# Kernel optimization log

Hardware: AMD Instinct MI355X
Metric: run time of the kernel (lower is better)

The kernel has to match this reference:

```python
import jax, jax.numpy as jnp
import numpy as np

B, L, H = 2, 512, 128

def setup_inputs() -> dict:
    key = jax.random.key(0)
    k1, k2, k3, _ = jax.random.split(key, 4)
    x = jax.random.normal(k1, (B, L, H), jnp.float32)
    y = jax.random.normal(k2, (B, L, H), jnp.float32)
    W_weight = jax.random.normal(k3, (H, 3 * H), jnp.float32) / np.sqrt(3 * H).astype(np.float32)
    W_bias = jnp.zeros((H,), jnp.float32)
    return {"x": x, "y": y, "W_weight": W_weight, "W_bias": W_bias}

def _span_max_context(x):
    """context[b,i,j,h] = max_{k=min(i,j)..max(i,j)} x[b,k,h], shape [B,L,L,H].
    Equivalent to the torch loop of diagonal running-max + symmetric scatter."""
    Bb, Ll, Hh = x.shape
    neg = jnp.full((Bb, 1, Hh), -jnp.inf, x.dtype)
    x_pad = jnp.concatenate([x, neg], axis=1)              # [B,L+1,H]
    d = jnp.arange(Ll)[:, None]                            # diagonal offset
    j = jnp.arange(Ll)[None, :]                            # start position
    shift_idx = jnp.minimum(d + j, Ll)                     # [L,L]; L -> -inf pad
    X2 = x_pad[:, shift_idx, :]                            # X2[b,d,j] = x[b,j+d]
    D = jax.lax.cummax(X2, axis=1)                         # D[b,d,j] = max_{k=j..j+d} x[b,k]
    i = jnp.arange(Ll)[:, None]
    jj = jnp.arange(Ll)[None, :]
    off = jnp.abs(i - jj)                                  # |i-j|
    lo = jnp.minimum(i, jj)                                # min(i,j)
    return D[:, off, lo, :]                                # [B,L,L,H]

def reference(x, y, W_weight, W_bias):
    Hh = x.shape[-1]
    ctx = _span_max_context(x)
    # Split W over the concat [x_i, y_j, context_ij] to avoid a [B,L,L,3H] intermediate.
    Wx, Wy, Wc = W_weight[:, :Hh], W_weight[:, Hh:2 * Hh], W_weight[:, 2 * Hh:]
    t = (jnp.einsum('blh,gh->blg', x, Wx)[:, :, None, :]
         + jnp.einsum('blh,gh->blg', y, Wy)[:, None, :, :]
         + jnp.einsum('bijh,gh->bijg', ctx, Wc)
         + W_bias)
    return jax.nn.gelu(t, approximate=False)               # [B,L,L,H]
```

## Files before the change

kernel.cpp:

```cpp
#include <hip/hip_runtime.h>
#include <hip/hip_bf16.h>

#define LL 512
#define HH 128
#define NBATCH 2
#define NT 32
#define NOFF (NT*(NT-1)/2)

typedef float f32x4 __attribute__((ext_vector_type(4)));
typedef short s16x8 __attribute__((ext_vector_type(8)));
typedef unsigned int u32x4 __attribute__((ext_vector_type(4)));

__device__ __forceinline__ unsigned short f2bfu(float f){
  __hip_bfloat16 h = __float2bfloat16(f);
  return __builtin_bit_cast(unsigned short, h);
}
__device__ __forceinline__ unsigned int bmax2(unsigned int a, unsigned int b){
  float lo = fmaxf(__uint_as_float(a << 16), __uint_as_float(b << 16));
  float hi = fmaxf(__uint_as_float(a & 0xFFFF0000u), __uint_as_float(b & 0xFFFF0000u));
  return __float_as_uint(hi) | (__float_as_uint(lo) >> 16);
}
__device__ __forceinline__ unsigned int packbf2(float lo, float hi){
  return ((__float_as_uint(hi) + 0x8000u) & 0xFFFF0000u)
       | ((__float_as_uint(lo) + 0x8000u) >> 16);
}
__device__ __forceinline__ u32x4 bmax4(u32x4 a, u32x4 b){
  u32x4 r; r[0]=bmax2(a[0],b[0]); r[1]=bmax2(a[1],b[1]);
  r[2]=bmax2(a[2],b[2]); r[3]=bmax2(a[3],b[3]); return r;
}
__device__ __forceinline__ float gelu_f(float v){
  float inner = v * fmaf(0.044715f, v*v, 1.0f);
  float e = __expf(1.5957691216f * inner);
  float s = __fdividef(1.0f, e + 1.0f);
  return fmaf(-v, s, v);
}
__device__ __forceinline__ f32x4 gelu4(f32x4 v){
  f32x4 r;
  #pragma unroll
  for (int i=0;i<4;++i) r[i] = gelu_f(v[i]);
  return r;
}

__global__ void prep_kernel(const float* __restrict__ x, const float* __restrict__ y,
                            const float* __restrict__ W, const float* __restrict__ bias,
                            float* __restrict__ t1, float* __restrict__ t2,
                            float* __restrict__ bmax, short* __restrict__ Wcb){
  int blk = blockIdx.x, tid = threadIdx.x;
  if (blk < NBATCH*LL){
    int b = blk >> 9, l = blk & (LL-1);
    __shared__ float xs[HH], ys[HH];
    size_t base = ((size_t)b*LL + l)*HH;
    if (tid < HH) xs[tid] = x[base + tid];
    else          ys[tid-HH] = y[base + tid - HH];
    __syncthreads();
    int role = tid >> 7, g = tid & (HH-1);
    const float4* wr = (const float4*)(W + (size_t)g*384 + role*HH);
    const float4* vs = (const float4*)(role ? ys : xs);
    float sA = 0.f, sB = 0.f;
    #pragma unroll
    for (int q=0;q<32;q+=2){
      float4 a = vs[q],   w1 = wr[q];
      sA = fmaf(a.x,w1.x, fmaf(a.y,w1.y, fmaf(a.z,w1.z, fmaf(a.w,w1.w, sA))));
      float4 c = vs[q+1], w2 = wr[q+1];
      sB = fmaf(c.x,w2.x, fmaf(c.y,w2.y, fmaf(c.z,w2.z, fmaf(c.w,w2.w, sB))));
    }
    float s = sA + sB;
    if (role == 0) t1[base + g] = s + bias[g];
    else           t2[base + g] = s;
  } else if (blk < NBATCH*LL + NBATCH*NT/2){
    int e = (blk - NBATCH*LL)*2 + (tid >> 7);
    int h = tid & (HH-1);
    int b = e >> 5, t = e & 31;
    float m = -INFINITY;
    #pragma unroll
    for (int r=0;r<16;++r) m = fmaxf(m, x[((size_t)b*LL + t*16 + r)*HH + h]);
    bmax[(size_t)e*HH + h] = m;
  } else {
    int e0 = ((blk - (NBATCH*LL + NBATCH*NT/2))*256 + tid)*8;
    #pragma unroll
    for (int i=0;i<8;++i){
      int e = e0 + i; int g = e >> 7, h = e & (HH-1);
      Wcb[e] = (short)f2bfu(W[(size_t)g*384 + 256 + h]);
    }
  }
}

__global__ __launch_bounds__(256, 4) void ctx_kernel(
    const float* __restrict__ x, const float* __restrict__ t1,
    const float* __restrict__ t2, const float* __restrict__ bmax,
    const short* __restrict__ Wcb, float* __restrict__ out)
{
  __shared__ __align__(16) unsigned int shs[8192];
  const int tid = threadIdx.x;
  const int b = blockIdx.y;
  const int w = tid >> 6, l = tid & 63, l16 = l & 15, lhi = l >> 4;
  const size_t bL = (size_t)b*LL;
  float* Bw = (float*)shs + w*1024;
  unsigned short* sIU = (unsigned short*)(shs + 4096);
  unsigned short* sJU = sIU + 2048;
  unsigned short* M   = (unsigned short*)(shs + 4096);

  const bool isdiag = (blockIdx.x >= NOFF);
  int ti, tj;
  if (!isdiag){
    int rem = blockIdx.x; ti = 0;
    while (rem >= NT-1-ti){ rem -= NT-1-ti; ++ti; }
    tj = ti + 1 + rem;
  } else { ti = tj = blockIdx.x - NOFF; }

  if (!isdiag){
    int role = tid >> 7, h = tid & (HH-1);
    if (role == 0){
      const float* xp = x + (bL + ti*16)*HH + h;
      float run = -INFINITY;
      #pragma unroll
      for (int r=15;r>=0;--r){ run = fmaxf(run, xp[r*HH]);
        sIU[r*HH + (h ^ ((r&7)<<3))] = f2bfu(run); }
    } else {
      const float* bp = bmax + ((size_t)b*NT)*HH + h;
      float run = -INFINITY;
      for (int t=ti+1;t<tj;++t) run = fmaxf(run, bp[t*HH]);
      const float* xp = x + (bL + tj*16)*HH + h;
      #pragma unroll
      for (int r=0;r<16;++r){ run = fmaxf(run, xp[r*HH]);
        sJU[r*HH + (h ^ ((r&7)<<3))] = f2bfu(run); }
    }
    __syncthreads();
  } else {
    { int e = tid*8; int r = e >> 7, h0 = e & (HH-1);
      const float* xp = x + (bL + ti*16 + r)*HH + h0;
      f32x4 v0 = *(const f32x4*)xp, v1 = *(const f32x4*)(xp+4);
      u32x4 pk; pk[0]=packbf2(v0[0],v0[1]); pk[1]=packbf2(v0[2],v0[3]);
      pk[2]=packbf2(v1[0],v1[1]); pk[3]=packbf2(v1[2],v1[3]);
      *(u32x4*)&M[r*HH + (h0 ^ ((r&7)<<3))] = pk;
    }
    __syncthreads();
    #pragma unroll
    for (int k=1;k<4;++k){
      int e = tid*8; int r = e >> 7, h0 = e & (HH-1);
      int r2 = min(r + (1<<(k-1)), 15);
      u32x4 a = *(const u32x4*)&M[((k-1)*16 + r )*HH + (h0 ^ ((r &7)<<3))];
      u32x4 c = *(const u32x4*)&M[((k-1)*16 + r2)*HH + (h0 ^ ((r2&7)<<3))];
      *(u32x4*)&M[(k*16 + r)*HH + (h0 ^ ((r&7)<<3))] = bmax4(a, c);
      __syncthreads();
    }
  }

  const int i0 = ti*16, j0 = tj*16;

  #pragma unroll
  for (int ps=0; ps<2; ++ps){
    const int ptA = w*4 + ps*2;
    u32x4 fr[2][4];
    if (!isdiag){
      #pragma unroll
      for (int s=0;s<2;++s){
        int pt = ptA + s;
        #pragma unroll
        for (int kb=0;kb<4;++kb){
          int h0 = kb*32 + lhi*8;
          u32x4 si = *(const u32x4*)&sIU[pt*HH + (h0 ^ ((pt&7)<<3))];
          u32x4 pj = *(const u32x4*)&sJU[l16*HH + (h0 ^ ((l16&7)<<3))];
          fr[s][kb] = bmax4(si, pj);
        }
      }
    } else {
      #pragma unroll
      for (int s=0;s<2;++s){
        int pt = ptA + s;
        int a = min(pt, l16), bb2 = max(pt, l16);
        int len = bb2 - a + 1;
        int k = 31 - __clz(len); if (k>3) k=3;
        int r2 = bb2 + 1 - (1<<k);
        #pragma unroll
        for (int kb=0;kb<4;++kb){
          int h0 = kb*32 + lhi*8;
          u32x4 ua = *(const u32x4*)&M[(k*16+a )*HH + (h0 ^ ((a &7)<<3))];
          u32x4 ub = *(const u32x4*)&M[(k*16+r2)*HH + (h0 ^ ((r2&7)<<3))];
          fr[s][kb] = bmax4(ua, ub);
        }
      }
    }

    #pragma unroll
    for (int q4=0; q4<4; ++q4){
      #pragma unroll
      for (int hf=0; hf<2; ++hf){
        const int nt = q4*2 + hf;
        s16x8 wcf[4];
        #pragma unroll
        for (int kb=0;kb<4;++kb)
          wcf[kb] = *(const s16x8*)(Wcb + (size_t)(nt*16+l16)*HH + kb*32 + lhi*8);
        f32x4 a0 = (f32x4){0.f,0.f,0.f,0.f}, a1 = a0;
        #pragma unroll
        for (int kb=0;kb<4;++kb){
          a0 = __builtin_amdgcn_mfma_f32_16x16x32_bf16(wcf[kb],
                 __builtin_bit_cast(s16x8, fr[0][kb]), a0, 0, 0, 0);
          a1 = __builtin_amdgcn_mfma_f32_16x16x32_bf16(wcf[kb],
                 __builtin_bit_cast(s16x8, fr[1][kb]), a1, 0, 0, 0);
        }
        const int wo = (hf*16 + lhi*4) ^ ((l16&7)<<2);
        *(f32x4*)&Bw[      l16*32 + wo] = a0;
        *(f32x4*)&Bw[512 + l16*32 + wo] = a1;
      }
      asm volatile("" ::: "memory");

      const int gq = q4*32 + (l&7)*4;
      #pragma unroll
      for (int s=0;s<2;++s){
        const int irow = i0 + ptA + s;
        f32x4 t1i = *(const f32x4*)(t1 + (bL+irow)*HH + gq);
        #pragma unroll
        for (int it=0; it<2; ++it){
          const int j = it*8 + (l>>3);
          f32x4 v = *(const f32x4*)&Bw[s*512 + j*32 + (((l&7)*4) ^ ((j&7)<<2))];
          f32x4 t2j = *(const f32x4*)(t2 + (bL+j0+j)*HH + gq);
          *(f32x4*)(out + ((bL+irow)*LL + j0+j)*HH + gq) = gelu4(v + t1i + t2j);
        }
      }
      if (!isdiag){
        const int s2 = (l>>3)&1;
        const int icol = i0 + ptA + s2;
        f32x4 t2i = *(const f32x4*)(t2 + (bL+icol)*HH + gq);
        #pragma unroll
        for (int it=0; it<4; ++it){
          const int j = it*4 + (l>>4);
          f32x4 v = *(const f32x4*)&Bw[s2*512 + j*32 + (((l&7)*4) ^ ((j&7)<<2))];
          f32x4 t1j = *(const f32x4*)(t1 + (bL+j0+j)*HH + gq);
          *(f32x4*)(out + ((bL+j0+j)*LL + icol)*HH + gq) = gelu4(v + t1j + t2i);
        }
      }
      asm volatile("" ::: "memory");
    }
  }
}

extern "C" void kernel_launch(void* const* d_in, const int* in_sizes, int n_in,
                              void* d_out, int out_size, void* d_ws, size_t ws_size,
                              hipStream_t stream) {
  const float* x    = (const float*)d_in[0];
  const float* y    = (const float*)d_in[1];
  const float* W    = (const float*)d_in[2];
  const float* bias = (const float*)d_in[3];
  float* out = (float*)d_out;

  float* t1 = (float*)d_ws;
  float* t2 = t1 + (size_t)NBATCH*LL*HH;
  float* bmax = t2 + (size_t)NBATCH*LL*HH;
  short* Wcb = (short*)(bmax + (size_t)NBATCH*NT*HH);

  prep_kernel<<<NBATCH*LL + NBATCH*NT/2 + 8, 256, 0, stream>>>(x, y, W, bias, t1, t2, bmax, Wcb);
  ctx_kernel<<<dim3(NOFF + NT, NBATCH), 256, 0, stream>>>(x, t1, t2, bmax, Wcb, out);
}
```

Baseline: 98.00 us.

## Restructure context kernel to one row per block with precomputed tile prefix/suffix maxima

```diff
diff --git a/kernel.cpp b/kernel.cpp
--- a/kernel.cpp
+++ b/kernel.cpp
@@ -5,7 +5,6 @@
 #define HH 128
 #define NBATCH 2
 #define NT 32
-#define NOFF (NT*(NT-1)/2)
 
 typedef float f32x4 __attribute__((ext_vector_type(4)));
 typedef short s16x8 __attribute__((ext_vector_type(8)));
@@ -19,10 +18,6 @@
   float lo = fmaxf(__uint_as_float(a << 16), __uint_as_float(b << 16));
   float hi = fmaxf(__uint_as_float(a & 0xFFFF0000u), __uint_as_float(b & 0xFFFF0000u));
   return __float_as_uint(hi) | (__float_as_uint(lo) >> 16);
-}
-__device__ __forceinline__ unsigned int packbf2(float lo, float hi){
-  return ((__float_as_uint(hi) + 0x8000u) & 0xFFFF0000u)
-       | ((__float_as_uint(lo) + 0x8000u) >> 16);
 }
 __device__ __forceinline__ u32x4 bmax4(u32x4 a, u32x4 b){
   u32x4 r; r[0]=bmax2(a[0],b[0]); r[1]=bmax2(a[1],b[1]);
@@ -44,7 +39,8 @@
 __global__ void prep_kernel(const float* __restrict__ x, const float* __restrict__ y,
                             const float* __restrict__ W, const float* __restrict__ bias,
                             float* __restrict__ t1, float* __restrict__ t2,
-                            float* __restrict__ bmax, short* __restrict__ Wcb){
+                            float* __restrict__ tilemax, short* __restrict__ pfxT,
+                            short* __restrict__ sfxT, short* __restrict__ Wcb){
   int blk = blockIdx.x, tid = threadIdx.x;
   if (blk < NBATCH*LL){
     int b = blk >> 9, l = blk & (LL-1);
@@ -67,16 +63,25 @@
     float s = sA + sB;
     if (role == 0) t1[base + g] = s + bias[g];
     else           t2[base + g] = s;
-  } else if (blk < NBATCH*LL + NBATCH*NT/2){
-    int e = (blk - NBATCH*LL)*2 + (tid >> 7);
-    int h = tid & (HH-1);
+  } else if (blk < NBATCH*LL + NBATCH*NT){
+    int e = blk - NBATCH*LL;
     int b = e >> 5, t = e & 31;
-    float m = -INFINITY;
-    #pragma unroll
-    for (int r=0;r<16;++r) m = fmaxf(m, x[((size_t)b*LL + t*16 + r)*HH + h]);
-    bmax[(size_t)e*HH + h] = m;
+    int role = tid >> 7, h = tid & (HH-1);
+    const float* xp = x + ((size_t)b*LL + t*16)*HH + h;
+    if (role == 0){
+      float run = -INFINITY;
+      #pragma unroll
+      for (int r=0;r<16;++r){ run = fmaxf(run, xp[r*HH]);
+        pfxT[(((size_t)b*NT + t)*16 + r)*HH + h] = (short)f2bfu(run); }
+      tilemax[((size_t)b*NT + t)*HH + h] = run;
+    } else {
+      float run = -INFINITY;
+      #pragma unroll
+      for (int r=15;r>=0;--r){ run = fmaxf(run, xp[r*HH]);
+        sfxT[(((size_t)b*NT + t)*16 + r)*HH + h] = (short)f2bfu(run); }
+    }
   } else {
-    int e0 = ((blk - (NBATCH*LL + NBATCH*NT/2))*256 + tid)*8;
+    int e0 = ((blk - (NBATCH*LL + NBATCH*NT))*256 + tid)*8;
     #pragma unroll
     for (int i=0;i<8;++i){
       int e = e0 + i; int g = e >> 7, h = e & (HH-1);
@@ -87,150 +92,104 @@
 
 __global__ __launch_bounds__(256, 4) void ctx_kernel(
     const float* __restrict__ x, const float* __restrict__ t1,
-    const float* __restrict__ t2, const float* __restrict__ bmax,
+    const float* __restrict__ t2, const float* __restrict__ tilemax,
+    const short* __restrict__ pfxT, const short* __restrict__ sfxT,
     const short* __restrict__ Wcb, float* __restrict__ out)
 {
-  __shared__ __align__(16) unsigned int shs[8192];
+  __shared__ __align__(16) float ownT[16][HH];
+  __shared__ __align__(16) unsigned short chainU[NT*HH];
+  __shared__ __align__(16) unsigned short ownCU[16*HH];
+
   const int tid = threadIdx.x;
-  const int b = blockIdx.y;
+  const int i = blockIdx.x, b = blockIdx.y;
+  const int ti = i >> 4, ri = i & 15;
+  const size_t bL = (size_t)b*LL;
+
+  {
+    int r = tid >> 4, c0 = (tid & 15)*8;
+    const f32x4* sp = (const f32x4*)(x + (bL + ti*16 + r)*HH + c0);
+    *(f32x4*)&ownT[r][c0]   = sp[0];
+    *(f32x4*)&ownT[r][c0+4] = sp[1];
+  }
+  __syncthreads();
+
+  {
+    int role = tid >> 7, h = tid & (HH-1);
+    const float* tm = tilemax + ((size_t)b*NT)*HH + h;
+    if (role == 0){
+      float s = -INFINITY;
+      for (int r=ri; r<16; ++r) s = fmaxf(s, ownT[r][h]);
+      float run = s;
+      for (int t=ti+1; t<NT; ++t){
+        chainU[t*HH + h] = f2bfu(run);
+        run = fmaxf(run, tm[(size_t)t*HH]);
+      }
+      float r2 = ownT[ri][h];
+      ownCU[ri*HH + (h ^ ((ri&7)<<3))] = f2bfu(r2);
+      for (int jr=ri+1; jr<16; ++jr){
+        r2 = fmaxf(r2, ownT[jr][h]);
+        ownCU[jr*HH + (h ^ ((jr&7)<<3))] = f2bfu(r2);
+      }
+    } else {
+      float p = -INFINITY;
+      for (int r=0; r<=ri; ++r) p = fmaxf(p, ownT[r][h]);
+      float run = p;
+      for (int t=ti-1; t>=0; --t){
+        chainU[t*HH + h] = f2bfu(run);
+        run = fmaxf(run, tm[(size_t)t*HH]);
+      }
+      float r2 = ownT[ri][h];
+      for (int jr=ri-1; jr>=0; --jr){
+        r2 = fmaxf(r2, ownT[jr][h]);
+        ownCU[jr*HH + (h ^ ((jr&7)<<3))] = f2bfu(r2);
+      }
+    }
+  }
+  __syncthreads();
+
   const int w = tid >> 6, l = tid & 63, l16 = l & 15, lhi = l >> 4;
-  const size_t bL = (size_t)b*LL;
-  float* Bw = (float*)shs + w*1024;
-  unsigned short* sIU = (unsigned short*)(shs + 4096);
-  unsigned short* sJU = sIU + 2048;
-  unsigned short* M   = (unsigned short*)(shs + 4096);
-
-  const bool isdiag = (blockIdx.x >= NOFF);
-  int ti, tj;
-  if (!isdiag){
-    int rem = blockIdx.x; ti = 0;
-    while (rem >= NT-1-ti){ rem -= NT-1-ti; ++ti; }
-    tj = ti + 1 + rem;
-  } else { ti = tj = blockIdx.x - NOFF; }
-
-  if (!isdiag){
-    int role = tid >> 7, h = tid & (HH-1);
-    if (role == 0){
-      const float* xp = x + (bL + ti*16)*HH + h;
-      float run = -INFINITY;
-      #pragma unroll
-      for (int r=15;r>=0;--r){ run = fmaxf(run, xp[r*HH]);
-        sIU[r*HH + (h ^ ((r&7)<<3))] = f2bfu(run); }
-    } else {
-      const float* bp = bmax + ((size_t)b*NT)*HH + h;
-      float run = -INFINITY;
-      for (int t=ti+1;t<tj;++t) run = fmaxf(run, bp[t*HH]);
-      const float* xp = x + (bL + tj*16)*HH + h;
-      #pragma unroll
-      for (int r=0;r<16;++r){ run = fmaxf(run, xp[r*HH]);
-        sJU[r*HH + (h ^ ((r&7)<<3))] = f2bfu(run); }
-    }
-    __syncthreads();
-  } else {
-    { int e = tid*8; int r = e >> 7, h0 = e & (HH-1);
-      const float* xp = x + (bL + ti*16 + r)*HH + h0;
-      f32x4 v0 = *(const f32x4*)xp, v1 = *(const f32x4*)(xp+4);
-      u32x4 pk; pk[0]=packbf2(v0[0],v0[1]); pk[1]=packbf2(v0[2],v0[3]);
-      pk[2]=packbf2(v1[0],v1[1]); pk[3]=packbf2(v1[2],v1[3]);
-      *(u32x4*)&M[r*HH + (h0 ^ ((r&7)<<3))] = pk;
-    }
-    __syncthreads();
-    #pragma unroll
-    for (int k=1;k<4;++k){
-      int e = tid*8; int r = e >> 7, h0 = e & (HH-1);
-      int r2 = min(r + (1<<(k-1)), 15);
-      u32x4 a = *(const u32x4*)&M[((k-1)*16 + r )*HH + (h0 ^ ((r &7)<<3))];
-      u32x4 c = *(const u32x4*)&M[((k-1)*16 + r2)*HH + (h0 ^ ((r2&7)<<3))];
-      *(u32x4*)&M[(k*16 + r)*HH + (h0 ^ ((r&7)<<3))] = bmax4(a, c);
-      __syncthreads();
-    }
-  }
-
-  const int i0 = ti*16, j0 = tj*16;
 
   #pragma unroll
-  for (int ps=0; ps<2; ++ps){
-    const int ptA = w*4 + ps*2;
-    u32x4 fr[2][4];
-    if (!isdiag){
-      #pragma unroll
-      for (int s=0;s<2;++s){
-        int pt = ptA + s;
+  for (int grp=0; grp<2; ++grp){
+    const int tbase = w*8 + grp*4;
+    u32x4 fr[4][4];
+    #pragma unroll
+    for (int tt=0; tt<4; ++tt){
+      const int t = tbase + tt;
+      #pragma unroll
+      for (int kb=0; kb<4; ++kb){
+        const int h0 = kb*32 + lhi*8;
+        u32x4 f;
+        if (t == ti){
+          f = *(const u32x4*)&ownCU[l16*HH + (h0 ^ ((l16&7)<<3))];
+        } else {
+          u32x4 c = *(const u32x4*)&chainU[t*HH + h0];
+          const short* side = (t > ti) ? pfxT : sfxT;
+          u32x4 p = *(const u32x4*)&side[(((size_t)b*NT + t)*16 + l16)*HH + h0];
+          f = bmax4(p, c);
+        }
+        fr[tt][kb] = f;
+      }
+    }
+    #pragma unroll
+    for (int nt=0; nt<8; ++nt){
+      s16x8 wcf[4];
+      #pragma unroll
+      for (int kb=0; kb<4; ++kb)
+        wcf[kb] = *(const s16x8*)(Wcb + (size_t)(nt*16 + l16)*HH + kb*32 + lhi*8);
+      const int gg = nt*16 + lhi*4;
+      f32x4 t1v = *(const f32x4*)(t1 + (bL + i)*HH + gg);
+      #pragma unroll
+      for (int tt=0; tt<4; ++tt){
+        f32x4 acc = (f32x4){0.f,0.f,0.f,0.f};
         #pragma unroll
-        for (int kb=0;kb<4;++kb){
-          int h0 = kb*32 + lhi*8;
-          u32x4 si = *(const u32x4*)&sIU[pt*HH + (h0 ^ ((pt&7)<<3))];
-          u32x4 pj = *(const u32x4*)&sJU[l16*HH + (h0 ^ ((l16&7)<<3))];
-          fr[s][kb] = bmax4(si, pj);
-        }
-      }
-    } else {
-      #pragma unroll
-      for (int s=0;s<2;++s){
-        int pt = ptA + s;
-        int a = min(pt, l16), bb2 = max(pt, l16);
-        int len = bb2 - a + 1;
-        int k = 31 - __clz(len); if (k>3) k=3;
-        int r2 = bb2 + 1 - (1<<k);
-        #pragma unroll
-        for (int kb=0;kb<4;++kb){
-          int h0 = kb*32 + lhi*8;
-          u32x4 ua = *(const u32x4*)&M[(k*16+a )*HH + (h0 ^ ((a &7)<<3))];
-          u32x4 ub = *(const u32x4*)&M[(k*16+r2)*HH + (h0 ^ ((r2&7)<<3))];
-          fr[s][kb] = bmax4(ua, ub);
-        }
-      }
-    }
-
-    #pragma unroll
-    for (int q4=0; q4<4; ++q4){
-      #pragma unroll
-      for (int hf=0; hf<2; ++hf){
-        const int nt = q4*2 + hf;
-        s16x8 wcf[4];
-        #pragma unroll
-        for (int kb=0;kb<4;++kb)
-          wcf[kb] = *(const s16x8*)(Wcb + (size_t)(nt*16+l16)*HH + kb*32 + lhi*8);
-        f32x4 a0 = (f32x4){0.f,0.f,0.f,0.f}, a1 = a0;
-        #pragma unroll
-        for (int kb=0;kb<4;++kb){
-          a0 = __builtin_amdgcn_mfma_f32_16x16x32_bf16(wcf[kb],
-                 __builtin_bit_cast(s16x8, fr[0][kb]), a0, 0, 0, 0);
-          a1 = __builtin_amdgcn_mfma_f32_16x16x32_bf16(wcf[kb],
-                 __builtin_bit_cast(s16x8, fr[1][kb]), a1, 0, 0, 0);
-        }
-        const int wo = (hf*16 + lhi*4) ^ ((l16&7)<<2);
-        *(f32x4*)&Bw[      l16*32 + wo] = a0;
-        *(f32x4*)&Bw[512 + l16*32 + wo] = a1;
-      }
-      asm volatile("" ::: "memory");
-
-      const int gq = q4*32 + (l&7)*4;
-      #pragma unroll
-      for (int s=0;s<2;++s){
-        const int irow = i0 + ptA + s;
-        f32x4 t1i = *(const f32x4*)(t1 + (bL+irow)*HH + gq);
-        #pragma unroll
-        for (int it=0; it<2; ++it){
-          const int j = it*8 + (l>>3);
-          f32x4 v = *(const f32x4*)&Bw[s*512 + j*32 + (((l&7)*4) ^ ((j&7)<<2))];
-          f32x4 t2j = *(const f32x4*)(t2 + (bL+j0+j)*HH + gq);
-          *(f32x4*)(out + ((bL+irow)*LL + j0+j)*HH + gq) = gelu4(v + t1i + t2j);
-        }
-      }
-      if (!isdiag){
-        const int s2 = (l>>3)&1;
-        const int icol = i0 + ptA + s2;
-        f32x4 t2i = *(const f32x4*)(t2 + (bL+icol)*HH + gq);
-        #pragma unroll
-        for (int it=0; it<4; ++it){
-          const int j = it*4 + (l>>4);
-          f32x4 v = *(const f32x4*)&Bw[s2*512 + j*32 + (((l&7)*4) ^ ((j&7)<<2))];
-          f32x4 t1j = *(const f32x4*)(t1 + (bL+j0+j)*HH + gq);
-          *(f32x4*)(out + ((bL+j0+j)*LL + icol)*HH + gq) = gelu4(v + t1j + t2i);
-        }
-      }
-      asm volatile("" ::: "memory");
+        for (int kb=0; kb<4; ++kb)
+          acc = __builtin_amdgcn_mfma_f32_16x16x32_bf16(wcf[kb],
+                  __builtin_bit_cast(s16x8, fr[tt][kb]), acc, 0, 0, 0);
+        const int j = (tbase + tt)*16 + l16;
+        f32x4 t2v = *(const f32x4*)(t2 + (bL + j)*HH + gg);
+        *(f32x4*)(out + ((bL + i)*LL + j)*HH + gg) = gelu4(acc + t1v + t2v);
+      }
     }
   }
 }
@@ -244,11 +203,15 @@
   const float* bias = (const float*)d_in[3];
   float* out = (float*)d_out;
 
-  float* t1 = (float*)d_ws;
-  float* t2 = t1 + (size_t)NBATCH*LL*HH;
-  float* bmax = t2 + (size_t)NBATCH*LL*HH;
-  short* Wcb = (short*)(bmax + (size_t)NBATCH*NT*HH);
-
-  prep_kernel<<<NBATCH*LL + NBATCH*NT/2 + 8, 256, 0, stream>>>(x, y, W, bias, t1, t2, bmax, Wcb);
-  ctx_kernel<<<dim3(NOFF + NT, NBATCH), 256, 0, stream>>>(x, t1, t2, bmax, Wcb, out);
-}
+  float* t1      = (float*)d_ws;
+  float* t2      = t1 + (size_t)NBATCH*LL*HH;
+  float* tilemax = t2 + (size_t)NBATCH*LL*HH;
+  short* Wcb  = (short*)(tilemax + (size_t)NBATCH*NT*HH);
+  short* pfxT = Wcb + (size_t)HH*HH;
+  short* sfxT = pfxT + (size_t)NBATCH*NT*16*HH;
+
+  prep_kernel<<<NBATCH*LL + NBATCH*NT + 8, 256, 0, stream>>>(
+      x, y, W, bias, t1, t2, tilemax, pfxT, sfxT, Wcb);
+  ctx_kernel<<<dim3(LL, NBATCH), 256, 0, stream>>>(
+      x, t1, t2, tilemax, pfxT, sfxT, Wcb, out);
+}
```

Result: slower. 139.9 us (+42.8%).
